# Optimization experiments

Hardware: AMD Instinct MI355X
Metric: run time of the kernel (lower is better)

## Reference

```python
import jax, jax.numpy as jnp
import numpy as np

B, T, D_MODEL, WINDOW = 2, 2048, 512, 32


def setup_inputs() -> dict:
    key = jax.random.key(0)
    ks = jax.random.split(key, 5)
    s = 1.0 / np.sqrt(D_MODEL)
    x = jax.random.normal(ks[0], (B, T, D_MODEL), jnp.float32)
    # torch.nn.Linear convention: weight [out_features, in_features], y = x @ W.T + b
    w_qkv = jax.random.uniform(ks[1], (3 * D_MODEL, D_MODEL), jnp.float32, -s, s)
    b_qkv = jax.random.uniform(ks[2], (3 * D_MODEL,), jnp.float32, -s, s)
    w_proj = jax.random.uniform(ks[3], (D_MODEL, D_MODEL), jnp.float32, -s, s)
    b_proj = jax.random.uniform(ks[4], (D_MODEL,), jnp.float32, -s, s)
    return {"x": x, "w_qkv": w_qkv, "b_qkv": b_qkv, "w_proj": w_proj, "b_proj": b_proj}


def reference(x, w_qkv, b_qkv, w_proj, b_proj):
    Bb, Tt, C = x.shape
    qkv = x @ w_qkv.T + b_qkv                      # [B,T,3C]
    q, k, v = jnp.split(qkv, 3, axis=-1)           # each [B,T,C]
    W = 2 * WINDOW - 1                             # non-causal window span [t-w+1, t+w-1]
    offs = jnp.arange(W) - (WINDOW - 1)            # [W]
    idx = jnp.arange(Tt)[:, None] + offs[None, :]  # [T,W] absolute key positions
    valid = (idx >= 0) & (idx < Tt)                # mask out-of-range window slots
    idx_c = jnp.clip(idx, 0, Tt - 1)
    k_win = k[:, idx_c]                            # [B,T,W,C]
    v_win = v[:, idx_c]                            # [B,T,W,C]
    scale = jnp.asarray(C, x.dtype) ** 0.5
    scores = jnp.einsum('btc,btwc->btw', q, k_win) / scale
    scores = jnp.where(valid[None], scores, -jnp.inf)
    p = jax.nn.softmax(scores, axis=-1)            # [B,T,W]
    out = jnp.einsum('btw,btwc->btc', p, v_win)    # [B,T,C]
    return out @ w_proj.T + b_proj
```

## Files before the change

kernel.cpp:

```cpp
#include <hip/hip_runtime.h>
#include <math.h>

#define BB 2
#define TT 2048
#define CC 512
#define WIN 32
#define WSZ 63
#define MM (BB * TT)

typedef __attribute__((ext_vector_type(8))) short short8;
typedef __attribute__((ext_vector_type(4))) float floatx4;

__device__ inline unsigned short bf16_rn(float f) {
  unsigned u = __builtin_bit_cast(unsigned, f);
  u += 0x7fff + ((u >> 16) & 1);
  return (unsigned short)(u >> 16);
}
__device__ inline unsigned pack_bf16x2(float lo, float hi) {
  return (unsigned)bf16_rn(lo) | ((unsigned)bf16_rn(hi) << 16);
}

__device__ inline void gll16(const void* g, void* l) {
  __builtin_amdgcn_global_load_lds(
      (const __attribute__((address_space(1))) void*)g,
      (__attribute__((address_space(3))) void*)l, 16, 0, 0);
}

#define NX  (MM * CC)
#define NWQ (3 * CC * CC)
#define NWP (CC * CC)

__global__ __launch_bounds__(256) void convert_bf16(
    const float* __restrict__ x, const float* __restrict__ wq,
    const float* __restrict__ wp, ushort* __restrict__ xb,
    ushort* __restrict__ wqb, ushort* __restrict__ wpb) {
  const size_t e = ((size_t)blockIdx.x * 256 + threadIdx.x) * 8;
  const float* src;
  ushort* dst;
  size_t off;
  if (e < NX) { src = x; dst = xb; off = e; }
  else if (e < NX + NWQ) { src = wq; dst = wqb; off = e - NX; }
  else { src = wp; dst = wpb; off = e - NX - NWQ; }
  float4 v0 = ((const float4*)(src + off))[0];
  float4 v1 = ((const float4*)(src + off))[1];
  uint4 o;
  o.x = pack_bf16x2(v0.x, v0.y);
  o.y = pack_bf16x2(v0.z, v0.w);
  o.z = pack_bf16x2(v1.x, v1.y);
  o.w = pack_bf16x2(v1.z, v1.w);
  *(uint4*)(dst + off) = o;
}

#define GBK 32
#define VTBASE 1024

template <int BN, typename OT>
__global__ __launch_bounds__(256) void gemm_nt_mfma(
    const ushort* __restrict__ A, const ushort* __restrict__ B,
    const float* __restrict__ bias, OT* __restrict__ C,
    ushort* __restrict__ VT, int M, int N, int K) {
  constexpr int MI = 4;
  constexpr int NI = (BN == 128) ? 4 : 4;
  constexpr int MIW = (BN == 128) ? 4 : 2;
  __shared__ __align__(16) ushort As[128 * GBK];
  __shared__ __align__(16) ushort Bs[BN * GBK];

  const int tid = threadIdx.x;
  const int lane = tid & 63;
  const int wave = tid >> 6;
  const int wm = (BN == 128) ? (wave >> 1) * 64 : wave * 32;
  const int wn = (BN == 128) ? (wave & 1) * 64 : 0;
  const int m0 = blockIdx.y * 128;
  const int n0 = blockIdx.x * BN;
  const int mlane = lane & 15, quad = lane >> 4;
  const int lrow = lane >> 2, lcol = (lane & 3) * 8;

  floatx4 acc[MIW][NI];
#pragma unroll
  for (int i = 0; i < MIW; ++i)
#pragma unroll
    for (int j = 0; j < NI; ++j) acc[i][j] = (floatx4){0.f, 0.f, 0.f, 0.f};

  for (int k0 = 0; k0 < K; k0 += GBK) {
    __syncthreads();
#pragma unroll
    for (int q = 0; q < 2; ++q) {
      const int r0 = (q * 4 + wave) * 16;
      gll16(A + (size_t)(m0 + r0 + lrow) * K + k0 + lcol, As + r0 * GBK);
    }
#pragma unroll
    for (int q = 0; q < BN / 64; ++q) {
      const int r0 = (q * 4 + wave) * 16;
      gll16(B + (size_t)(n0 + r0 + lrow) * K + k0 + lcol, Bs + r0 * GBK);
    }
    __syncthreads();

    short8 af[MIW], bfr[NI];
#pragma unroll
    for (int mi = 0; mi < MIW; ++mi)
      af[mi] = *(const short8*)(&As[(wm + mi * 16 + mlane) * GBK + quad * 8]);
#pragma unroll
    for (int ni = 0; ni < NI; ++ni)
      bfr[ni] = *(const short8*)(&Bs[(wn + ni * 16 + mlane) * GBK + quad * 8]);
#pragma unroll
    for (int mi = 0; mi < MIW; ++mi)
#pragma unroll
      for (int ni = 0; ni < NI; ++ni)
        acc[mi][ni] = __builtin_amdgcn_mfma_f32_16x16x32_bf16(af[mi], bfr[ni], acc[mi][ni], 0, 0, 0);
  }

  const bool vpath = (VT != nullptr) && (n0 >= VTBASE);
#pragma unroll
  for (int ni = 0; ni < NI; ++ni) {
    const int n = n0 + wn + ni * 16 + mlane;
    const float bn = bias[n];
#pragma unroll
    for (int mi = 0; mi < MIW; ++mi) {
      const int mbase = m0 + wm + mi * 16 + quad * 4;
      if (vpath) {
        ushort4 pk;
        pk.x = bf16_rn(acc[mi][ni][0] + bn);
        pk.y = bf16_rn(acc[mi][ni][1] + bn);
        pk.z = bf16_rn(acc[mi][ni][2] + bn);
        pk.w = bf16_rn(acc[mi][ni][3] + bn);
        *(ushort4*)(VT + (size_t)(n - VTBASE) * M + mbase) = pk;
      } else {
#pragma unroll
        for (int r = 0; r < 4; ++r) {
          float val = acc[mi][ni][r] + bn;
          if constexpr (sizeof(OT) == 2)
            ((ushort*)C)[(size_t)(mbase + r) * N + n] = bf16_rn(val);
          else
            ((float*)C)[(size_t)(mbase + r) * N + n] = val;
        }
      }
    }
  }
}

#define ATILE 16
#define NR 80
#define KLD 264
#define VLD 104
#define SLD 84
#define PLD 104

__global__ __launch_bounds__(256) void attn_mfma(
    const ushort* __restrict__ qkv, const ushort* __restrict__ vT,
    ushort* __restrict__ out) {
  __shared__ __align__(16) char smem[61952];
  ushort* kv_s = (ushort*)smem;
  ushort* q_s  = (ushort*)(smem + 42240);
  ushort* vt_s = (ushort*)smem;
  float*  s_s  = (float*)(smem + 53248);
  ushort* p_s  = (ushort*)(smem + 58624);

  const int tid = threadIdx.x;
  const int wave = tid >> 6, lane = tid & 63;
  const int mlane = lane & 15, quad = lane >> 4;
  const int bt0 = blockIdx.x * ATILE;
  const int b = bt0 / TT, t0 = bt0 % TT;
  const size_t rowbase = (size_t)b * TT * (3 * CC);

  floatx4 sacc0 = (floatx4){0.f, 0.f, 0.f, 0.f};
  floatx4 sacc1 = (floatx4){0.f, 0.f, 0.f, 0.f};

  for (int h = 0; h < 2; ++h) {
    if (h) __syncthreads();
#pragma unroll
    for (int i = 0; i < 2; ++i) {
      const int idx = tid + 256 * i;
      const int row = idx >> 5, cb = idx & 31;
      *(uint4*)(&q_s[row * KLD + cb * 8]) =
          *(const uint4*)(&qkv[rowbase + (size_t)(t0 + row) * (3 * CC) + h * 256 + cb * 8]);
    }
    for (int idx = tid; idx < NR * 32; idx += 256) {
      const int r = idx >> 5, cb = idx & 31;
      const int src = t0 - 32 + r;
      uint4 v = make_uint4(0, 0, 0, 0);
      if (src >= 0 && src < TT)
        v = *(const uint4*)(&qkv[rowbase + (size_t)src * (3 * CC) + CC + h * 256 + cb * 8]);
      *(uint4*)(&kv_s[r * KLD + cb * 8]) = v;
    }
    __syncthreads();
#pragma unroll
    for (int ks = 0; ks < 8; ++ks) {
      short8 a = *(const short8*)(&q_s[mlane * KLD + ks * 32 + quad * 8]);
      short8 b0 = *(const short8*)(&kv_s[(wave * 16 + mlane) * KLD + ks * 32 + quad * 8]);
      sacc0 = __builtin_amdgcn_mfma_f32_16x16x32_bf16(a, b0, sacc0, 0, 0, 0);
      if (wave == 0) {
        short8 b1 = *(const short8*)(&kv_s[(64 + mlane) * KLD + ks * 32 + quad * 8]);
        sacc1 = __builtin_amdgcn_mfma_f32_16x16x32_bf16(a, b1, sacc1, 0, 0, 0);
      }
    }
  }

#pragma unroll
  for (int r = 0; r < 4; ++r)
    s_s[(quad * 4 + r) * SLD + wave * 16 + mlane] = sacc0[r];
  if (wave == 0) {
#pragma unroll
    for (int r = 0; r < 4; ++r)
      s_s[(quad * 4 + r) * SLD + 64 + mlane] = sacc1[r];
  }
  __syncthreads();

  {
    const int row = tid >> 4, li = tid & 15;
    const float inv_scale = 0.044194173824159216f;
    float e[5];
    float mx = -INFINITY;
#pragma unroll
    for (int i = 0; i < 5; ++i) {
      const int r = li + 16 * i;
      const int j = r - 1 - row;
      const int src = t0 - 32 + r;
      const bool valid = (j >= 0) && (j < WSZ) && (src >= 0) && (src < TT);
      e[i] = valid ? s_s[row * SLD + r] * inv_scale : -INFINITY;
      mx = fmaxf(mx, e[i]);
    }
    mx = fmaxf(mx, __shfl_xor(mx, 1)); mx = fmaxf(mx, __shfl_xor(mx, 2));
    mx = fmaxf(mx, __shfl_xor(mx, 4)); mx = fmaxf(mx, __shfl_xor(mx, 8));
    float sum = 0.f;
#pragma unroll
    for (int i = 0; i < 5; ++i) {
      e[i] = (e[i] == -INFINITY) ? 0.f : __expf(e[i] - mx);
      sum += e[i];
    }
    sum += __shfl_xor(sum, 1); sum += __shfl_xor(sum, 2);
    sum += __shfl_xor(sum, 4); sum += __shfl_xor(sum, 8);
    const float rs = 1.f / sum;
#pragma unroll
    for (int i = 0; i < 5; ++i)
      p_s[row * PLD + li + 16 * i] = bf16_rn(e[i] * rs);
    if (li < 8) {
      p_s[row * PLD + 80 + li] = 0;
      p_s[row * PLD + 88 + li] = 0;
      p_s[row * PLD + 96 + li] = 0;
    }
  }

  const int mcol0 = b * TT + t0 - 32;
  for (int h = 0; h < 2; ++h) {
    __syncthreads();
    for (int idx = tid; idx < 256 * 12; idx += 256) {
      const int c = idx / 12, ch = idx % 12;
      uint4 v = make_uint4(0, 0, 0, 0);
      if (ch < 10)
        v = *(const uint4*)(&vT[(size_t)(h * 256 + c) * MM + mcol0 + ch * 8]);
      *(uint4*)(&vt_s[c * VLD + ch * 8]) = v;
    }
    __syncthreads();

    floatx4 oacc[4];
#pragma unroll
    for (int i = 0; i < 4; ++i) oacc[i] = (floatx4){0.f, 0.f, 0.f, 0.f};
#pragma unroll
    for (int ks = 0; ks < 3; ++ks) {
      short8 a = *(const short8*)(&p_s[mlane * PLD + ks * 32 + quad * 8]);
#pragma unroll
      for (int i = 0; i < 4; ++i) {
        short8 bfv = *(const short8*)(&vt_s[((wave * 4 + i) * 16 + mlane) * VLD + ks * 32 + quad * 8]);
        oacc[i] = __builtin_amdgcn_mfma_f32_16x16x32_bf16(a, bfv, oacc[i], 0, 0, 0);
      }
    }
#pragma unroll
    for (int i = 0; i < 4; ++i) {
      const int c = h * 256 + (wave * 4 + i) * 16 + mlane;
#pragma unroll
      for (int r = 0; r < 4; ++r)
        out[(size_t)(bt0 + quad * 4 + r) * CC + c] = bf16_rn(oacc[i][r]);
    }
  }
}

extern "C" void kernel_launch(void* const* d_in, const int* in_sizes, int n_in,
                              void* d_out, int out_size, void* d_ws, size_t ws_size,
                              hipStream_t stream) {
  const float* x      = (const float*)d_in[0];
  const float* w_qkv  = (const float*)d_in[1];
  const float* b_qkv  = (const float*)d_in[2];
  const float* w_proj = (const float*)d_in[3];
  const float* b_proj = (const float*)d_in[4];
  float* outp = (float*)d_out;

  ushort* qkv   = (ushort*)d_ws;
  ushort* attn  = qkv + (size_t)MM * 3 * CC;
  ushort* xb    = attn + (size_t)MM * CC;
  ushort* wqb   = xb + (size_t)NX;
  ushort* wpb   = wqb + (size_t)NWQ;
  ushort* vTg   = wpb + (size_t)NWP;
  ushort* vT    = vTg + 64;

  convert_bf16<<<(NX + NWQ + NWP) / (256 * 8), 256, 0, stream>>>(x, w_qkv, w_proj, xb, wqb, wpb);
  {
    dim3 grid((3 * CC) / 128, MM / 128);
    gemm_nt_mfma<128, ushort><<<grid, 256, 0, stream>>>(xb, wqb, b_qkv, qkv, vT, MM, 3 * CC, CC);
  }
  attn_mfma<<<MM / ATILE, 256, 0, stream>>>(qkv, vT, attn);
  {
    dim3 grid(CC / 64, MM / 128);
    gemm_nt_mfma<64, float><<<grid, 256, 0, stream>>>(attn, wpb, b_proj, outp, nullptr, MM, CC, CC);
  }
}
```

Measured before the change: 123.2 us.

## Load Q/K/V attention operands directly from global, halve query tile

The attention kernel no longer stages Q, K and V^T tiles in shared memory. MFMA operands are read straight from global memory with out-of-range key rows left unguarded, and a workspace pad in front of qkv makes those boundary reads stay in bounds. The query tile shrinks from 16 to 8 rows, so the launch has twice as many blocks and a much smaller LDS footprint. Only half the MFMA rows are stored. The aim is to remove the LDS staging and barriers and raise occupancy, at the cost of redundant K/V global traffic and wasted MFMA work.

```diff
diff --git a/kernel.cpp b/kernel.cpp
--- a/kernel.cpp
+++ b/kernel.cpp
@@ -59,8 +59,7 @@
     const ushort* __restrict__ A, const ushort* __restrict__ B,
     const float* __restrict__ bias, OT* __restrict__ C,
     ushort* __restrict__ VT, int M, int N, int K) {
-  constexpr int MI = 4;
-  constexpr int NI = (BN == 128) ? 4 : 4;
+  constexpr int NI = 4;
   constexpr int MIW = (BN == 128) ? 4 : 2;
   __shared__ __align__(16) ushort As[128 * GBK];
   __shared__ __align__(16) ushort Bs[BN * GBK];
@@ -138,60 +137,36 @@
   }
 }
 
-#define ATILE 16
-#define NR 80
-#define KLD 264
-#define VLD 104
+#define ATILE 8
 #define SLD 84
 #define PLD 104
 
 __global__ __launch_bounds__(256) void attn_mfma(
     const ushort* __restrict__ qkv, const ushort* __restrict__ vT,
     ushort* __restrict__ out) {
-  __shared__ __align__(16) char smem[61952];
-  ushort* kv_s = (ushort*)smem;
-  ushort* q_s  = (ushort*)(smem + 42240);
-  ushort* vt_s = (ushort*)smem;
-  float*  s_s  = (float*)(smem + 53248);
-  ushort* p_s  = (ushort*)(smem + 58624);
+  __shared__ __align__(16) float s_s[16 * SLD];
+  __shared__ __align__(16) ushort p_s[16 * PLD];
 
   const int tid = threadIdx.x;
   const int wave = tid >> 6, lane = tid & 63;
   const int mlane = lane & 15, quad = lane >> 4;
   const int bt0 = blockIdx.x * ATILE;
   const int b = bt0 / TT, t0 = bt0 % TT;
-  const size_t rowbase = (size_t)b * TT * (3 * CC);
-
+  const ushort* qbase = qkv + (size_t)b * TT * (3 * CC);
+
+  const ushort* qrow  = qbase + (ptrdiff_t)(t0 + mlane) * (3 * CC);
+  const ushort* krow0 = qbase + (ptrdiff_t)(t0 - 32 + wave * 16 + mlane) * (3 * CC) + CC;
+  const ushort* krow1 = qbase + (ptrdiff_t)(t0 - 32 + 64 + mlane) * (3 * CC) + CC;
   floatx4 sacc0 = (floatx4){0.f, 0.f, 0.f, 0.f};
   floatx4 sacc1 = (floatx4){0.f, 0.f, 0.f, 0.f};
-
-  for (int h = 0; h < 2; ++h) {
-    if (h) __syncthreads();
-#pragma unroll
-    for (int i = 0; i < 2; ++i) {
-      const int idx = tid + 256 * i;
-      const int row = idx >> 5, cb = idx & 31;
-      *(uint4*)(&q_s[row * KLD + cb * 8]) =
-          *(const uint4*)(&qkv[rowbase + (size_t)(t0 + row) * (3 * CC) + h * 256 + cb * 8]);
-    }
-    for (int idx = tid; idx < NR * 32; idx += 256) {
-      const int r = idx >> 5, cb = idx & 31;
-      const int src = t0 - 32 + r;
-      uint4 v = make_uint4(0, 0, 0, 0);
-      if (src >= 0 && src < TT)
-        v = *(const uint4*)(&qkv[rowbase + (size_t)src * (3 * CC) + CC + h * 256 + cb * 8]);
-      *(uint4*)(&kv_s[r * KLD + cb * 8]) = v;
-    }
-    __syncthreads();
-#pragma unroll
-    for (int ks = 0; ks < 8; ++ks) {
-      short8 a = *(const short8*)(&q_s[mlane * KLD + ks * 32 + quad * 8]);
-      short8 b0 = *(const short8*)(&kv_s[(wave * 16 + mlane) * KLD + ks * 32 + quad * 8]);
-      sacc0 = __builtin_amdgcn_mfma_f32_16x16x32_bf16(a, b0, sacc0, 0, 0, 0);
-      if (wave == 0) {
-        short8 b1 = *(const short8*)(&kv_s[(64 + mlane) * KLD + ks * 32 + quad * 8]);
-        sacc1 = __builtin_amdgcn_mfma_f32_16x16x32_bf16(a, b1, sacc1, 0, 0, 0);
-      }
+#pragma unroll
+  for (int ks = 0; ks < 16; ++ks) {
+    short8 a  = *(const short8*)(qrow + ks * 32 + quad * 8);
+    short8 b0 = *(const short8*)(krow0 + ks * 32 + quad * 8);
+    sacc0 = __builtin_amdgcn_mfma_f32_16x16x32_bf16(a, b0, sacc0, 0, 0, 0);
+    if (wave == 0) {
+      short8 b1 = *(const short8*)(krow1 + ks * 32 + quad * 8);
+      sacc1 = __builtin_amdgcn_mfma_f32_16x16x32_bf16(a, b1, sacc1, 0, 0, 0);
     }
   }
 
@@ -239,37 +214,24 @@
       p_s[row * PLD + 96 + li] = 0;
     }
   }
-
-  const int mcol0 = b * TT + t0 - 32;
-  for (int h = 0; h < 2; ++h) {
-    __syncthreads();
-    for (int idx = tid; idx < 256 * 12; idx += 256) {
-      const int c = idx / 12, ch = idx % 12;
-      uint4 v = make_uint4(0, 0, 0, 0);
-      if (ch < 10)
-        v = *(const uint4*)(&vT[(size_t)(h * 256 + c) * MM + mcol0 + ch * 8]);
-      *(uint4*)(&vt_s[c * VLD + ch * 8]) = v;
-    }
-    __syncthreads();
-
-    floatx4 oacc[4];
-#pragma unroll
-    for (int i = 0; i < 4; ++i) oacc[i] = (floatx4){0.f, 0.f, 0.f, 0.f};
+  __syncthreads();
+
+  const ptrdiff_t mcol0 = (ptrdiff_t)b * TT + t0 - 32;
+#pragma unroll 2
+  for (int nt8 = 0; nt8 < 8; ++nt8) {
+    const int nt = wave * 8 + nt8;
+    const ushort* vrow = vT + (ptrdiff_t)(nt * 16 + mlane) * MM + mcol0;
+    floatx4 o = (floatx4){0.f, 0.f, 0.f, 0.f};
 #pragma unroll
     for (int ks = 0; ks < 3; ++ks) {
-      short8 a = *(const short8*)(&p_s[mlane * PLD + ks * 32 + quad * 8]);
-#pragma unroll
-      for (int i = 0; i < 4; ++i) {
-        short8 bfv = *(const short8*)(&vt_s[((wave * 4 + i) * 16 + mlane) * VLD + ks * 32 + quad * 8]);
-        oacc[i] = __builtin_amdgcn_mfma_f32_16x16x32_bf16(a, bfv, oacc[i], 0, 0, 0);
-      }
-    }
-#pragma unroll
-    for (int i = 0; i < 4; ++i) {
-      const int c = h * 256 + (wave * 4 + i) * 16 + mlane;
+      short8 a  = *(const short8*)(&p_s[mlane * PLD + ks * 32 + quad * 8]);
+      short8 bv = *(const short8*)(vrow + ks * 32 + quad * 8);
+      o = __builtin_amdgcn_mfma_f32_16x16x32_bf16(a, bv, o, 0, 0, 0);
+    }
+    if (quad < 2) {
 #pragma unroll
       for (int r = 0; r < 4; ++r)
-        out[(size_t)(bt0 + quad * 4 + r) * CC + c] = bf16_rn(oacc[i][r]);
+        out[(size_t)(bt0 + quad * 4 + r) * CC + nt * 16 + mlane] = bf16_rn(o[r]);
     }
   }
 }
@@ -284,7 +246,8 @@
   const float* b_proj = (const float*)d_in[4];
   float* outp = (float*)d_out;
 
-  ushort* qkv   = (ushort*)d_ws;
+  ushort* base  = (ushort*)d_ws;
+  ushort* qkv   = base + 131072;
   ushort* attn  = qkv + (size_t)MM * 3 * CC;
   ushort* xb    = attn + (size_t)MM * CC;
   ushort* wqb   = xb + (size_t)NX;
```

Result: faster. 120.5 us (-2.2%).
